# Performance work log

Hardware: AMD Instinct MI355X
Metric: run time of the kernel (lower is better)

Reference implementation:

```python
import jax, jax.numpy as jnp
import numpy as np

EPS = 1e-05
FACT = 2.0
REJECT_RATIO = 1.0
B, N1, N2 = 8, 4096, 4096


def setup_inputs() -> dict:
    key = jax.random.key(0)
    k1, k2 = jax.random.split(key)
    pc1 = jax.random.normal(k1, (B, 4, N1), dtype=jnp.float32)
    pc2 = jax.random.normal(k2, (B, 4, N2), dtype=jnp.float32)
    # homogeneous coordinates: last row is 1
    pc1 = pc1.at[:, 3, :].set(1.0)
    pc2 = pc2.at[:, 3, :].set(1.0)
    return {"pc1": pc1, "pc2": pc2}


def _rot_to_quat(R):
    # quaternion [w, x, y, z] from 3x3 rotation matrix (branchless)
    def s(x):
        return jnp.where(x >= 0, 1.0, -1.0)
    qw = 0.5 * jnp.sqrt(jnp.maximum(1.0 + R[0, 0] + R[1, 1] + R[2, 2], 1e-12))
    qx = 0.5 * jnp.sqrt(jnp.maximum(1.0 + R[0, 0] - R[1, 1] - R[2, 2], 1e-12)) * s(R[2, 1] - R[1, 2])
    qy = 0.5 * jnp.sqrt(jnp.maximum(1.0 - R[0, 0] + R[1, 1] - R[2, 2], 1e-12)) * s(R[0, 2] - R[2, 0])
    qz = 0.5 * jnp.sqrt(jnp.maximum(1.0 - R[0, 0] - R[1, 1] + R[2, 2], 1e-12)) * s(R[1, 0] - R[0, 1])
    return jnp.stack([qw, qx, qy, qz])


def _single(pc1, pc2):
    # pc1: [4, N1], pc2: [4, N2]
    p1, p2 = pc1[:3], pc2[:3]
    # squared pairwise distance via matmul-expansion trick: [N1, N2]
    d = (jnp.sum(p1 ** 2, axis=0)[:, None]
         - 2.0 * jnp.einsum('dn,dm->nm', p1, p2)
         + jnp.sum(p2 ** 2, axis=0)[None, :])
    # soft nearest neighbor: softmax over N2 of fact / clamp(d, eps)
    w = jax.nn.softmax(FACT / jnp.maximum(d, EPS), axis=1)  # [N1, N2]
    pc_nearest = jnp.einsum('cm,nm->cn', pc2, w)            # [4, N1]

    # soft outlier rejection (near-hard threshold via steep sigmoid)
    dist = jnp.linalg.norm(pc1 - pc_nearest, axis=0)        # [N1]
    mean_dist = jnp.mean(dist)
    indexor = jax.nn.sigmoid((dist - mean_dist * REJECT_RATIO - EPS) * -1e10)

    # weighted Procrustes (soft_tf); note indexor weights BOTH centred clouds
    wsum = jnp.sum(indexor)
    c2 = jnp.sum(pc_nearest[:3] * indexor, axis=-1) / wsum  # [3]
    c1 = jnp.sum(pc1[:3] * indexor, axis=-1) / wsum         # [3]
    p2c = ((pc_nearest[:3] - c2[:, None]) * indexor).T      # [N1, 3]
    p1c = ((pc1[:3] - c1[:, None]) * indexor).T             # [N1, 3]
    H = p1c.T @ p2c                                         # [3, 3]
    U, S, Vh = jnp.linalg.svd(H, full_matrices=False)
    V = Vh.T
    sign = jnp.where(jnp.linalg.det(U) * jnp.linalg.det(V) < 0, -1.0, 1.0)
    V = V * jnp.array([1.0, 1.0, 1.0]).at[2].set(sign)[None, :]  # flip 3rd column
    R = V @ U.T
    t = c2 - R @ c1
    T = jnp.zeros((4, 4), dtype=pc1.dtype)
    T = T.at[:3, :3].set(R).at[:3, 3].set(t).at[3, 3].set(1.0)
    q = _rot_to_quat(R)
    return T, q, t


def reference(pc1, pc2):
    T, q, t = jax.vmap(_single)(pc1, pc2)
    return T, q, t
```

## Files before the change

### kernel.cpp

```cpp
#include <hip/hip_runtime.h>
#include <math.h>


typedef float v2f __attribute__((ext_vector_type(2)));

constexpr int cB  = 8;
constexpr int cN1 = 4096;
constexpr int cN2 = 4096;
constexpr int cMC = 8;
constexpr int cCHUNK = cN2 / cMC;
constexpr float cEPS  = 1e-5f;
constexpr float cKK   = 0.34657359027997264f;
constexpr float cEPSK = cEPS * cKK;
constexpr float cUNSC = -1.4426950408889634f;

constexpr size_t OFF_PARTM = 0x400000;
constexpr size_t OFF_NEAR  = 0x500000;

__global__ __launch_bounds__(256) void cpnet_partial(
    const float* __restrict__ pc1, const float* __restrict__ pc2,
    float4* __restrict__ partA, float* __restrict__ partM) {
  __shared__ float xs[cCHUNK], ys[cCHUNK], zs[cCHUNK], ws[cCHUNK];
  const int tid = threadIdx.x;
  const int b = blockIdx.z, c = blockIdx.y;
  const int n = blockIdx.x * 256 + tid;

  const float* p2b = pc2 + (size_t)b * 4 * cN2 + c * cCHUNK;
  for (int i = tid; i < cCHUNK; i += 256) {
    float x = p2b[i], y = p2b[cN2 + i], z = p2b[2 * cN2 + i];
    xs[i] = -2.0f * cKK * x;
    ys[i] = -2.0f * cKK * y;
    zs[i] = -2.0f * cKK * z;
    ws[i] = cKK * (x * x + y * y + z * z);
  }
  __syncthreads();

  const float* p1b = pc1 + (size_t)b * 4 * cN1;
  const float x1 = p1b[n], y1 = p1b[cN1 + n], z1 = p1b[2 * cN1 + n];
  const float n1k = cKK * (x1 * x1 + y1 * y1 + z1 * z1);
  const v2f X1 = {x1, x1}, Y1 = {y1, y1}, Z1 = {z1, z1}, N1K = {n1k, n1k};

  const v2f* xs2 = (const v2f*)xs;
  const v2f* ys2 = (const v2f*)ys;
  const v2f* zs2 = (const v2f*)zs;
  const v2f* ws2 = (const v2f*)ws;

  v2f dmin2 = {3.0e38f, 3.0e38f};
#pragma unroll 4
  for (int m = 0; m < cCHUNK / 2; ++m) {
    v2f dk = X1 * xs2[m] + (Y1 * ys2[m] + (Z1 * zs2[m] + (ws2[m] + N1K)));
    dmin2 = __builtin_elementwise_min(dmin2, dk);
  }
  const float dmin = fminf(dmin2.x, dmin2.y);
  const float M = __builtin_amdgcn_rcpf(fmaxf(dmin, cEPSK));
  const v2f M2 = {M, M};
  const v2f EPS2 = {cEPSK, cEPSK};

  v2f S2 = {0.f, 0.f}, Ax2 = {0.f, 0.f}, Ay2 = {0.f, 0.f}, Az2 = {0.f, 0.f};
#pragma unroll 4
  for (int m = 0; m < cCHUNK / 2; ++m) {
    v2f vx = xs2[m], vy = ys2[m], vz = zs2[m];
    v2f dk = X1 * vx + (Y1 * vy + (Z1 * vz + (ws2[m] + N1K)));
    dk = __builtin_elementwise_max(dk, EPS2);
    v2f s2v;
    s2v.x = __builtin_amdgcn_rcpf(dk.x);
    s2v.y = __builtin_amdgcn_rcpf(dk.y);
    v2f d2 = s2v - M2;
    v2f e;
    e.x = __builtin_amdgcn_exp2f(d2.x);
    e.y = __builtin_amdgcn_exp2f(d2.y);
    S2 += e;
    Ax2 += e * vx;
    Ay2 += e * vy;
    Az2 += e * vz;
  }

  const int idx = (c * cB + b) * cN1 + n;
  partA[idx] = make_float4(Ax2.x + Ax2.y, Ay2.x + Ay2.y, Az2.x + Az2.y,
                           S2.x + S2.y);
  partM[idx] = M;
}

__device__ __forceinline__ void reduce_multi(double* v, int nv, double* lds,
                                             int tid) {
  const int lane = tid & 63, w = tid >> 6;
  for (int i = 0; i < nv; ++i) {
    double x = v[i];
    for (int s = 32; s > 0; s >>= 1) x += __shfl_xor(x, s, 64);
    if (lane == 0) lds[i * 4 + w] = x;
  }
  __syncthreads();
  if (tid < nv)
    lds[tid * 4] = lds[tid * 4] + lds[tid * 4 + 1] + lds[tid * 4 + 2] +
                   lds[tid * 4 + 3];
  __syncthreads();
  for (int i = 0; i < nv; ++i) v[i] = lds[i * 4];
  __syncthreads();
}

__global__ __launch_bounds__(256) void cpnet_finalize(
    const float* __restrict__ pc1,
    const float4* __restrict__ partA, const float* __restrict__ partM,
    float4* __restrict__ near4, float* __restrict__ out) {
  const int b = blockIdx.x, tid = threadIdx.x;
  __shared__ double lds[32 * 4];

  const float* p1b = pc1 + (size_t)b * 4 * cN1;

  double acc[23];
  acc[0] = 0.0;
  for (int n = tid; n < cN1; n += 256) {
    float Ms[cMC];
    float g = -3.0e38f;
#pragma unroll
    for (int c = 0; c < cMC; ++c) {
      Ms[c] = partM[(c * cB + b) * cN1 + n];
      g = fmaxf(g, Ms[c]);
    }
    float S = 0.f, nx = 0.f, ny = 0.f, nz = 0.f;
#pragma unroll
    for (int c = 0; c < cMC; ++c) {
      float w = exp2f(Ms[c] - g);
      float4 a = partA[(c * cB + b) * cN1 + n];
      S += a.w * w; nx += a.x * w; ny += a.y * w; nz += a.z * w;
    }
    float inv = cUNSC / S;
    nx *= inv; ny *= inv; nz *= inv;
    float x1 = p1b[n], y1 = p1b[cN1 + n], z1 = p1b[2 * cN1 + n];
    float dx = x1 - nx, dy = y1 - ny, dz = z1 - nz;
    float dist = sqrtf(dx * dx + dy * dy + dz * dz);
    near4[b * cN1 + n] = make_float4(nx, ny, nz, dist);
    acc[0] += (double)dist;
  }
  reduce_multi(acc, 1, lds, tid);
  const float meanf = (float)(acc[0] / (double)cN1);

  for (int i = 0; i < 23; ++i) acc[i] = 0.0;
  for (int n = tid; n < cN1; n += 256) {
    float4 nn = near4[b * cN1 + n];
    float u = (nn.w - meanf - cEPS) * 1e10f;
    float ind = 1.0f / (1.0f + expf(u));
    double di = (double)ind, di2 = di * di;
    double x1 = (double)p1b[n], y1 = (double)p1b[cN1 + n],
           z1 = (double)p1b[2 * cN1 + n];
    double x2 = (double)nn.x, y2 = (double)nn.y, z2 = (double)nn.z;
    acc[0] += di;
    acc[1] += di * x1;  acc[2] += di * y1;  acc[3] += di * z1;
    acc[4] += di * x2;  acc[5] += di * y2;  acc[6] += di * z2;
    acc[7] += di2;
    acc[8] += di2 * x1;  acc[9] += di2 * y1;  acc[10] += di2 * z1;
    acc[11] += di2 * x2; acc[12] += di2 * y2; acc[13] += di2 * z2;
    acc[14] += di2 * x1 * x2; acc[15] += di2 * x1 * y2; acc[16] += di2 * x1 * z2;
    acc[17] += di2 * y1 * x2; acc[18] += di2 * y1 * y2; acc[19] += di2 * y1 * z2;
    acc[20] += di2 * z1 * x2; acc[21] += di2 * z1 * y2; acc[22] += di2 * z1 * z2;
  }
  reduce_multi(acc, 23, lds, tid);

  if (tid == 0) {
    double W = acc[0];
    double c1[3] = {acc[1] / W, acc[2] / W, acc[3] / W};
    double c2[3] = {acc[4] / W, acc[5] / W, acc[6] / W};
    double H[3][3];
    for (int i = 0; i < 3; ++i)
      for (int j = 0; j < 3; ++j)
        H[i][j] = acc[14 + 3 * i + j] - c2[j] * acc[8 + i] -
                  c1[i] * acc[11 + j] + c1[i] * c2[j] * acc[7];

    double trH = H[0][0] + H[1][1] + H[2][2];
    double Nm[4][4], V[4][4];
    Nm[0][0] = trH;
    Nm[0][1] = Nm[1][0] = H[1][2] - H[2][1];
    Nm[0][2] = Nm[2][0] = H[2][0] - H[0][2];
    Nm[0][3] = Nm[3][0] = H[0][1] - H[1][0];
    Nm[1][1] = 2.0 * H[0][0] - trH;
    Nm[1][2] = Nm[2][1] = H[0][1] + H[1][0];
    Nm[1][3] = Nm[3][1] = H[0][2] + H[2][0];
    Nm[2][2] = 2.0 * H[1][1] - trH;
    Nm[2][3] = Nm[3][2] = H[1][2] + H[2][1];
    Nm[3][3] = 2.0 * H[2][2] - trH;

    for (int i = 0; i < 4; ++i)
      for (int j = 0; j < 4; ++j) V[i][j] = (i == j) ? 1.0 : 0.0;

    for (int sweep = 0; sweep < 6; ++sweep) {
      for (int p = 0; p < 3; ++p) {
        for (int q = p + 1; q < 4; ++q) {
          double apq = Nm[p][q];
          if (fabs(apq) < 1e-300) continue;
          double theta = (Nm[q][q] - Nm[p][p]) / (2.0 * apq);
          double tt = (theta >= 0.0 ? 1.0 : -1.0) /
                      (fabs(theta) + sqrt(theta * theta + 1.0));
          double cc = 1.0 / sqrt(tt * tt + 1.0);
          double ss = tt * cc;
          for (int k = 0; k < 4; ++k) {
            double akp = Nm[k][p], akq = Nm[k][q];
            Nm[k][p] = cc * akp - ss * akq;
            Nm[k][q] = ss * akp + cc * akq;
          }
          for (int k = 0; k < 4; ++k) {
            double apk = Nm[p][k], aqk = Nm[q][k];
            Nm[p][k] = cc * apk - ss * aqk;
            Nm[q][k] = ss * apk + cc * aqk;
          }
          for (int k = 0; k < 4; ++k) {
            double vkp = V[k][p], vkq = V[k][q];
            V[k][p] = cc * vkp - ss * vkq;
            V[k][q] = ss * vkp + cc * vkq;
          }
        }
      }
    }
    int imax = 0;
    for (int i = 1; i < 4; ++i)
      if (Nm[i][i] > Nm[imax][imax]) imax = i;
    double qw = V[0][imax], qx = V[1][imax], qy = V[2][imax], qz = V[3][imax];
    double qn = sqrt(qw * qw + qx * qx + qy * qy + qz * qz);
    qw /= qn; qx /= qn; qy /= qn; qz /= qn;

    double R[3][3];
    R[0][0] = 1.0 - 2.0 * (qy * qy + qz * qz);
    R[0][1] = 2.0 * (qx * qy - qw * qz);
    R[0][2] = 2.0 * (qx * qz + qw * qy);
    R[1][0] = 2.0 * (qx * qy + qw * qz);
    R[1][1] = 1.0 - 2.0 * (qx * qx + qz * qz);
    R[1][2] = 2.0 * (qy * qz - qw * qx);
    R[2][0] = 2.0 * (qx * qz - qw * qy);
    R[2][1] = 2.0 * (qy * qz + qw * qx);
    R[2][2] = 1.0 - 2.0 * (qx * qx + qy * qy);

    double tr1 = 0.0, tr2 = 0.0;
    for (int i = 0; i < 3; ++i)
      for (int j = 0; j < 3; ++j) {
        tr1 += R[i][j] * H[j][i];
        tr2 += R[j][i] * H[j][i];
      }
    if (tr2 > tr1) {
      for (int i = 0; i < 3; ++i)
        for (int j = i + 1; j < 3; ++j) {
          double tmp = R[i][j]; R[i][j] = R[j][i]; R[j][i] = tmp;
        }
    }

    double tx = c2[0] - (R[0][0] * c1[0] + R[0][1] * c1[1] + R[0][2] * c1[2]);
    double ty = c2[1] - (R[1][0] * c1[0] + R[1][1] * c1[1] + R[1][2] * c1[2]);
    double tz = c2[2] - (R[2][0] * c1[0] + R[2][1] * c1[1] + R[2][2] * c1[2]);

    auto sgn = [](double x) { return x >= 0.0 ? 1.0 : -1.0; };
    double oqw = 0.5 * sqrt(fmax(1.0 + R[0][0] + R[1][1] + R[2][2], 1e-12));
    double oqx = 0.5 * sqrt(fmax(1.0 + R[0][0] - R[1][1] - R[2][2], 1e-12)) *
                 sgn(R[2][1] - R[1][2]);
    double oqy = 0.5 * sqrt(fmax(1.0 - R[0][0] + R[1][1] - R[2][2], 1e-12)) *
                 sgn(R[0][2] - R[2][0]);
    double oqz = 0.5 * sqrt(fmax(1.0 - R[0][0] - R[1][1] + R[2][2], 1e-12)) *
                 sgn(R[1][0] - R[0][1]);

    float* T = out + b * 16;
    T[0]  = (float)R[0][0]; T[1]  = (float)R[0][1]; T[2]  = (float)R[0][2]; T[3]  = (float)tx;
    T[4]  = (float)R[1][0]; T[5]  = (float)R[1][1]; T[6]  = (float)R[1][2]; T[7]  = (float)ty;
    T[8]  = (float)R[2][0]; T[9]  = (float)R[2][1]; T[10] = (float)R[2][2]; T[11] = (float)tz;
    T[12] = 0.f; T[13] = 0.f; T[14] = 0.f; T[15] = 1.f;
    float* Q = out + 128 + b * 4;
    Q[0] = (float)oqw; Q[1] = (float)oqx; Q[2] = (float)oqy; Q[3] = (float)oqz;
    float* Tt = out + 160 + b * 3;
    Tt[0] = (float)tx; Tt[1] = (float)ty; Tt[2] = (float)tz;
  }
}

extern "C" void kernel_launch(void* const* d_in, const int* in_sizes, int n_in,
                              void* d_out, int out_size, void* d_ws, size_t ws_size,
                              hipStream_t stream) {
  const float* pc1 = (const float*)d_in[0];
  const float* pc2 = (const float*)d_in[1];
  float* out = (float*)d_out;
  char* ws = (char*)d_ws;

  float4* partA  = (float4*)ws;
  float*  partM  = (float*)(ws + OFF_PARTM);
  float4* near4  = (float4*)(ws + OFF_NEAR);

  cpnet_partial<<<dim3(cN1 / 256, cMC, cB), 256, 0, stream>>>(pc1, pc2,
                                                              partA, partM);
  cpnet_finalize<<<cB, 256, 0, stream>>>(pc1, partA, partM, near4, out);
}
```

Before: 153.3 us.

## Split finalize into parallel combine, moments, and single-thread solve kernels

Replaces the 8-block finalize kernel with three kernels. The first two run on a 16x8 grid and combine the softmax partials and accumulate the weighted moments, each writing per-block partial sums to workspace. A tiny solve kernel then sums those partials and runs the Jacobi eigen solve. This spreads the serial per-batch reduction across many more CUs, at the cost of two extra kernel launches. The combined nearest-point data now overwrites chunk 0 of partA in place.

```diff
diff --git a/kernel.cpp b/kernel.cpp
--- a/kernel.cpp
+++ b/kernel.cpp
@@ -9,13 +9,15 @@
 constexpr int cN2 = 4096;
 constexpr int cMC = 8;
 constexpr int cCHUNK = cN2 / cMC;
+constexpr int cNB2 = cN1 / 256;
 constexpr float cEPS  = 1e-5f;
 constexpr float cKK   = 0.34657359027997264f;
 constexpr float cEPSK = cEPS * cKK;
 constexpr float cUNSC = -1.4426950408889634f;
 
 constexpr size_t OFF_PARTM = 0x400000;
-constexpr size_t OFF_NEAR  = 0x500000;
+constexpr size_t OFF_DPART = 0x500000;
+constexpr size_t OFF_MPART = 0x500400;
 
 __global__ __launch_bounds__(256) void cpnet_partial(
     const float* __restrict__ pc1, const float* __restrict__ pc2,
@@ -98,172 +100,198 @@
   __syncthreads();
 }
 
-__global__ __launch_bounds__(256) void cpnet_finalize(
-    const float* __restrict__ pc1,
-    const float4* __restrict__ partA, const float* __restrict__ partM,
-    float4* __restrict__ near4, float* __restrict__ out) {
-  const int b = blockIdx.x, tid = threadIdx.x;
+__global__ __launch_bounds__(256) void cpnet_combine(
+    const float* __restrict__ pc1, float4* partA,
+    const float* __restrict__ partM, double* __restrict__ dpart) {
   __shared__ double lds[32 * 4];
-
+  const int tid = threadIdx.x;
+  const int bx = blockIdx.x, b = blockIdx.y;
+  const int n = bx * 256 + tid;
+
+  float Ms[cMC];
+  float g = -3.0e38f;
+#pragma unroll
+  for (int c = 0; c < cMC; ++c) {
+    Ms[c] = partM[(c * cB + b) * cN1 + n];
+    g = fmaxf(g, Ms[c]);
+  }
+  float S = 0.f, nx = 0.f, ny = 0.f, nz = 0.f;
+#pragma unroll
+  for (int c = 0; c < cMC; ++c) {
+    float w = exp2f(Ms[c] - g);
+    float4 a = partA[(c * cB + b) * cN1 + n];
+    S += a.w * w; nx += a.x * w; ny += a.y * w; nz += a.z * w;
+  }
+  float inv = cUNSC / S;
+  nx *= inv; ny *= inv; nz *= inv;
   const float* p1b = pc1 + (size_t)b * 4 * cN1;
+  float dx = p1b[n] - nx, dy = p1b[cN1 + n] - ny, dz = p1b[2 * cN1 + n] - nz;
+  float dist = sqrtf(dx * dx + dy * dy + dz * dz);
+  partA[(0 * cB + b) * cN1 + n] = make_float4(nx, ny, nz, dist);
+
+  double acc[1];
+  acc[0] = (double)dist;
+  reduce_multi(acc, 1, lds, tid);
+  if (tid == 0) dpart[b * cNB2 + bx] = acc[0];
+}
+
+__global__ __launch_bounds__(256) void cpnet_moments(
+    const float* __restrict__ pc1, const float4* __restrict__ partA,
+    const double* __restrict__ dpart, double* __restrict__ mpart) {
+  __shared__ double lds[32 * 4];
+  const int tid = threadIdx.x;
+  const int bx = blockIdx.x, b = blockIdx.y;
+  const int n = bx * 256 + tid;
+
+  double dsum = 0.0;
+  for (int i = 0; i < cNB2; ++i) dsum += dpart[b * cNB2 + i];
+  const float meanf = (float)(dsum * (1.0 / (double)cN1));
+
+  float4 nn = partA[(0 * cB + b) * cN1 + n];
+  float u = (nn.w - meanf - cEPS) * 1e10f;
+  float ind = 1.0f / (1.0f + expf(u));
+  const float* p1b = pc1 + (size_t)b * 4 * cN1;
+  double di = (double)ind, di2 = di * di;
+  double x1 = (double)p1b[n], y1 = (double)p1b[cN1 + n],
+         z1 = (double)p1b[2 * cN1 + n];
+  double x2 = (double)nn.x, y2 = (double)nn.y, z2 = (double)nn.z;
+
+  double a[23];
+  a[0] = di;
+  a[1] = di * x1;  a[2] = di * y1;  a[3] = di * z1;
+  a[4] = di * x2;  a[5] = di * y2;  a[6] = di * z2;
+  a[7] = di2;
+  a[8]  = di2 * x1;  a[9]  = di2 * y1;  a[10] = di2 * z1;
+  a[11] = di2 * x2;  a[12] = di2 * y2;  a[13] = di2 * z2;
+  a[14] = di2 * x1 * x2; a[15] = di2 * x1 * y2; a[16] = di2 * x1 * z2;
+  a[17] = di2 * y1 * x2; a[18] = di2 * y1 * y2; a[19] = di2 * y1 * z2;
+  a[20] = di2 * z1 * x2; a[21] = di2 * z1 * y2; a[22] = di2 * z1 * z2;
+
+  reduce_multi(a, 23, lds, tid);
+  if (tid == 0) {
+    double* mb = mpart + (size_t)(b * cNB2 + bx) * 23;
+    for (int i = 0; i < 23; ++i) mb[i] = a[i];
+  }
+}
+
+__global__ __launch_bounds__(64) void cpnet_solve(
+    const double* __restrict__ mpart, float* __restrict__ out) {
+  const int b = blockIdx.x;
+  if (threadIdx.x != 0) return;
 
   double acc[23];
-  acc[0] = 0.0;
-  for (int n = tid; n < cN1; n += 256) {
-    float Ms[cMC];
-    float g = -3.0e38f;
-#pragma unroll
-    for (int c = 0; c < cMC; ++c) {
-      Ms[c] = partM[(c * cB + b) * cN1 + n];
-      g = fmaxf(g, Ms[c]);
-    }
-    float S = 0.f, nx = 0.f, ny = 0.f, nz = 0.f;
-#pragma unroll
-    for (int c = 0; c < cMC; ++c) {
-      float w = exp2f(Ms[c] - g);
-      float4 a = partA[(c * cB + b) * cN1 + n];
-      S += a.w * w; nx += a.x * w; ny += a.y * w; nz += a.z * w;
-    }
-    float inv = cUNSC / S;
-    nx *= inv; ny *= inv; nz *= inv;
-    float x1 = p1b[n], y1 = p1b[cN1 + n], z1 = p1b[2 * cN1 + n];
-    float dx = x1 - nx, dy = y1 - ny, dz = z1 - nz;
-    float dist = sqrtf(dx * dx + dy * dy + dz * dz);
-    near4[b * cN1 + n] = make_float4(nx, ny, nz, dist);
-    acc[0] += (double)dist;
-  }
-  reduce_multi(acc, 1, lds, tid);
-  const float meanf = (float)(acc[0] / (double)cN1);
-
   for (int i = 0; i < 23; ++i) acc[i] = 0.0;
-  for (int n = tid; n < cN1; n += 256) {
-    float4 nn = near4[b * cN1 + n];
-    float u = (nn.w - meanf - cEPS) * 1e10f;
-    float ind = 1.0f / (1.0f + expf(u));
-    double di = (double)ind, di2 = di * di;
-    double x1 = (double)p1b[n], y1 = (double)p1b[cN1 + n],
-           z1 = (double)p1b[2 * cN1 + n];
-    double x2 = (double)nn.x, y2 = (double)nn.y, z2 = (double)nn.z;
-    acc[0] += di;
-    acc[1] += di * x1;  acc[2] += di * y1;  acc[3] += di * z1;
-    acc[4] += di * x2;  acc[5] += di * y2;  acc[6] += di * z2;
-    acc[7] += di2;
-    acc[8] += di2 * x1;  acc[9] += di2 * y1;  acc[10] += di2 * z1;
-    acc[11] += di2 * x2; acc[12] += di2 * y2; acc[13] += di2 * z2;
-    acc[14] += di2 * x1 * x2; acc[15] += di2 * x1 * y2; acc[16] += di2 * x1 * z2;
-    acc[17] += di2 * y1 * x2; acc[18] += di2 * y1 * y2; acc[19] += di2 * y1 * z2;
-    acc[20] += di2 * z1 * x2; acc[21] += di2 * z1 * y2; acc[22] += di2 * z1 * z2;
-  }
-  reduce_multi(acc, 23, lds, tid);
-
-  if (tid == 0) {
-    double W = acc[0];
-    double c1[3] = {acc[1] / W, acc[2] / W, acc[3] / W};
-    double c2[3] = {acc[4] / W, acc[5] / W, acc[6] / W};
-    double H[3][3];
-    for (int i = 0; i < 3; ++i)
-      for (int j = 0; j < 3; ++j)
-        H[i][j] = acc[14 + 3 * i + j] - c2[j] * acc[8 + i] -
-                  c1[i] * acc[11 + j] + c1[i] * c2[j] * acc[7];
-
-    double trH = H[0][0] + H[1][1] + H[2][2];
-    double Nm[4][4], V[4][4];
-    Nm[0][0] = trH;
-    Nm[0][1] = Nm[1][0] = H[1][2] - H[2][1];
-    Nm[0][2] = Nm[2][0] = H[2][0] - H[0][2];
-    Nm[0][3] = Nm[3][0] = H[0][1] - H[1][0];
-    Nm[1][1] = 2.0 * H[0][0] - trH;
-    Nm[1][2] = Nm[2][1] = H[0][1] + H[1][0];
-    Nm[1][3] = Nm[3][1] = H[0][2] + H[2][0];
-    Nm[2][2] = 2.0 * H[1][1] - trH;
-    Nm[2][3] = Nm[3][2] = H[1][2] + H[2][1];
-    Nm[3][3] = 2.0 * H[2][2] - trH;
-
-    for (int i = 0; i < 4; ++i)
-      for (int j = 0; j < 4; ++j) V[i][j] = (i == j) ? 1.0 : 0.0;
-
-    for (int sweep = 0; sweep < 6; ++sweep) {
-      for (int p = 0; p < 3; ++p) {
-        for (int q = p + 1; q < 4; ++q) {
-          double apq = Nm[p][q];
-          if (fabs(apq) < 1e-300) continue;
-          double theta = (Nm[q][q] - Nm[p][p]) / (2.0 * apq);
-          double tt = (theta >= 0.0 ? 1.0 : -1.0) /
-                      (fabs(theta) + sqrt(theta * theta + 1.0));
-          double cc = 1.0 / sqrt(tt * tt + 1.0);
-          double ss = tt * cc;
-          for (int k = 0; k < 4; ++k) {
-            double akp = Nm[k][p], akq = Nm[k][q];
-            Nm[k][p] = cc * akp - ss * akq;
-            Nm[k][q] = ss * akp + cc * akq;
-          }
-          for (int k = 0; k < 4; ++k) {
-            double apk = Nm[p][k], aqk = Nm[q][k];
-            Nm[p][k] = cc * apk - ss * aqk;
-            Nm[q][k] = ss * apk + cc * aqk;
-          }
-          for (int k = 0; k < 4; ++k) {
-            double vkp = V[k][p], vkq = V[k][q];
-            V[k][p] = cc * vkp - ss * vkq;
-            V[k][q] = ss * vkp + cc * vkq;
-          }
+  for (int k = 0; k < cNB2; ++k) {
+    const double* mb = mpart + (size_t)(b * cNB2 + k) * 23;
+    for (int i = 0; i < 23; ++i) acc[i] += mb[i];
+  }
+
+  double W = acc[0];
+  double c1[3] = {acc[1] / W, acc[2] / W, acc[3] / W};
+  double c2[3] = {acc[4] / W, acc[5] / W, acc[6] / W};
+  double H[3][3];
+  for (int i = 0; i < 3; ++i)
+    for (int j = 0; j < 3; ++j)
+      H[i][j] = acc[14 + 3 * i + j] - c2[j] * acc[8 + i] -
+                c1[i] * acc[11 + j] + c1[i] * c2[j] * acc[7];
+
+  double trH = H[0][0] + H[1][1] + H[2][2];
+  double Nm[4][4], V[4][4];
+  Nm[0][0] = trH;
+  Nm[0][1] = Nm[1][0] = H[1][2] - H[2][1];
+  Nm[0][2] = Nm[2][0] = H[2][0] - H[0][2];
+  Nm[0][3] = Nm[3][0] = H[0][1] - H[1][0];
+  Nm[1][1] = 2.0 * H[0][0] - trH;
+  Nm[1][2] = Nm[2][1] = H[0][1] + H[1][0];
+  Nm[1][3] = Nm[3][1] = H[0][2] + H[2][0];
+  Nm[2][2] = 2.0 * H[1][1] - trH;
+  Nm[2][3] = Nm[3][2] = H[1][2] + H[2][1];
+  Nm[3][3] = 2.0 * H[2][2] - trH;
+
+  for (int i = 0; i < 4; ++i)
+    for (int j = 0; j < 4; ++j) V[i][j] = (i == j) ? 1.0 : 0.0;
+
+  for (int sweep = 0; sweep < 6; ++sweep) {
+    for (int p = 0; p < 3; ++p) {
+      for (int q = p + 1; q < 4; ++q) {
+        double apq = Nm[p][q];
+        if (fabs(apq) < 1e-300) continue;
+        double theta = (Nm[q][q] - Nm[p][p]) / (2.0 * apq);
+        double tt = (theta >= 0.0 ? 1.0 : -1.0) /
+                    (fabs(theta) + sqrt(theta * theta + 1.0));
+        double cc = 1.0 / sqrt(tt * tt + 1.0);
+        double ss = tt * cc;
+        for (int k = 0; k < 4; ++k) {
+          double akp = Nm[k][p], akq = Nm[k][q];
+          Nm[k][p] = cc * akp - ss * akq;
+          Nm[k][q] = ss * akp + cc * akq;
+        }
+        for (int k = 0; k < 4; ++k) {
+          double apk = Nm[p][k], aqk = Nm[q][k];
+          Nm[p][k] = cc * apk - ss * aqk;
+          Nm[q][k] = ss * apk + cc * aqk;
+        }
+        for (int k = 0; k < 4; ++k) {
+          double vkp = V[k][p], vkq = V[k][q];
+          V[k][p] = cc * vkp - ss * vkq;
+          V[k][q] = ss * vkp + cc * vkq;
         }
       }
     }
-    int imax = 0;
-    for (int i = 1; i < 4; ++i)
-      if (Nm[i][i] > Nm[imax][imax]) imax = i;
-    double qw = V[0][imax], qx = V[1][imax], qy = V[2][imax], qz = V[3][imax];
-    double qn = sqrt(qw * qw + qx * qx + qy * qy + qz * qz);
-    qw /= qn; qx /= qn; qy /= qn; qz /= qn;
-
-    double R[3][3];
-    R[0][0] = 1.0 - 2.0 * (qy * qy + qz * qz);
-    R[0][1] = 2.0 * (qx * qy - qw * qz);
-    R[0][2] = 2.0 * (qx * qz + qw * qy);
-    R[1][0] = 2.0 * (qx * qy + qw * qz);
-    R[1][1] = 1.0 - 2.0 * (qx * qx + qz * qz);
-    R[1][2] = 2.0 * (qy * qz - qw * qx);
-    R[2][0] = 2.0 * (qx * qz - qw * qy);
-    R[2][1] = 2.0 * (qy * qz + qw * qx);
-    R[2][2] = 1.0 - 2.0 * (qx * qx + qy * qy);
-
-    double tr1 = 0.0, tr2 = 0.0;
+  }
+  int imax = 0;
+  for (int i = 1; i < 4; ++i)
+    if (Nm[i][i] > Nm[imax][imax]) imax = i;
+  double qw = V[0][imax], qx = V[1][imax], qy = V[2][imax], qz = V[3][imax];
+  double qn = sqrt(qw * qw + qx * qx + qy * qy + qz * qz);
+  qw /= qn; qx /= qn; qy /= qn; qz /= qn;
+
+  double R[3][3];
+  R[0][0] = 1.0 - 2.0 * (qy * qy + qz * qz);
+  R[0][1] = 2.0 * (qx * qy - qw * qz);
+  R[0][2] = 2.0 * (qx * qz + qw * qy);
+  R[1][0] = 2.0 * (qx * qy + qw * qz);
+  R[1][1] = 1.0 - 2.0 * (qx * qx + qz * qz);
+  R[1][2] = 2.0 * (qy * qz - qw * qx);
+  R[2][0] = 2.0 * (qx * qz - qw * qy);
+  R[2][1] = 2.0 * (qy * qz + qw * qx);
+  R[2][2] = 1.0 - 2.0 * (qx * qx + qy * qy);
+
+  double tr1 = 0.0, tr2 = 0.0;
+  for (int i = 0; i < 3; ++i)
+    for (int j = 0; j < 3; ++j) {
+      tr1 += R[i][j] * H[j][i];
+      tr2 += R[j][i] * H[j][i];
+    }
+  if (tr2 > tr1) {
     for (int i = 0; i < 3; ++i)
-      for (int j = 0; j < 3; ++j) {
-        tr1 += R[i][j] * H[j][i];
-        tr2 += R[j][i] * H[j][i];
+      for (int j = i + 1; j < 3; ++j) {
+        double tmp = R[i][j]; R[i][j] = R[j][i]; R[j][i] = tmp;
       }
-    if (tr2 > tr1) {
-      for (int i = 0; i < 3; ++i)
-        for (int j = i + 1; j < 3; ++j) {
-          double tmp = R[i][j]; R[i][j] = R[j][i]; R[j][i] = tmp;
-        }
-    }
-
-    double tx = c2[0] - (R[0][0] * c1[0] + R[0][1] * c1[1] + R[0][2] * c1[2]);
-    double ty = c2[1] - (R[1][0] * c1[0] + R[1][1] * c1[1] + R[1][2] * c1[2]);
-    double tz = c2[2] - (R[2][0] * c1[0] + R[2][1] * c1[1] + R[2][2] * c1[2]);
-
-    auto sgn = [](double x) { return x >= 0.0 ? 1.0 : -1.0; };
-    double oqw = 0.5 * sqrt(fmax(1.0 + R[0][0] + R[1][1] + R[2][2], 1e-12));
-    double oqx = 0.5 * sqrt(fmax(1.0 + R[0][0] - R[1][1] - R[2][2], 1e-12)) *
-                 sgn(R[2][1] - R[1][2]);
-    double oqy = 0.5 * sqrt(fmax(1.0 - R[0][0] + R[1][1] - R[2][2], 1e-12)) *
-                 sgn(R[0][2] - R[2][0]);
-    double oqz = 0.5 * sqrt(fmax(1.0 - R[0][0] - R[1][1] + R[2][2], 1e-12)) *
-                 sgn(R[1][0] - R[0][1]);
-
-    float* T = out + b * 16;
-    T[0]  = (float)R[0][0]; T[1]  = (float)R[0][1]; T[2]  = (float)R[0][2]; T[3]  = (float)tx;
-    T[4]  = (float)R[1][0]; T[5]  = (float)R[1][1]; T[6]  = (float)R[1][2]; T[7]  = (float)ty;
-    T[8]  = (float)R[2][0]; T[9]  = (float)R[2][1]; T[10] = (float)R[2][2]; T[11] = (float)tz;
-    T[12] = 0.f; T[13] = 0.f; T[14] = 0.f; T[15] = 1.f;
-    float* Q = out + 128 + b * 4;
-    Q[0] = (float)oqw; Q[1] = (float)oqx; Q[2] = (float)oqy; Q[3] = (float)oqz;
-    float* Tt = out + 160 + b * 3;
-    Tt[0] = (float)tx; Tt[1] = (float)ty; Tt[2] = (float)tz;
-  }
+  }
+
+  double tx = c2[0] - (R[0][0] * c1[0] + R[0][1] * c1[1] + R[0][2] * c1[2]);
+  double ty = c2[1] - (R[1][0] * c1[0] + R[1][1] * c1[1] + R[1][2] * c1[2]);
+  double tz = c2[2] - (R[2][0] * c1[0] + R[2][1] * c1[1] + R[2][2] * c1[2]);
+
+  auto sgn = [](double x) { return x >= 0.0 ? 1.0 : -1.0; };
+  double oqw = 0.5 * sqrt(fmax(1.0 + R[0][0] + R[1][1] + R[2][2], 1e-12));
+  double oqx = 0.5 * sqrt(fmax(1.0 + R[0][0] - R[1][1] - R[2][2], 1e-12)) *
+               sgn(R[2][1] - R[1][2]);
+  double oqy = 0.5 * sqrt(fmax(1.0 - R[0][0] + R[1][1] - R[2][2], 1e-12)) *
+               sgn(R[0][2] - R[2][0]);
+  double oqz = 0.5 * sqrt(fmax(1.0 - R[0][0] - R[1][1] + R[2][2], 1e-12)) *
+               sgn(R[1][0] - R[0][1]);
+
+  float* T = out + b * 16;
+  T[0]  = (float)R[0][0]; T[1]  = (float)R[0][1]; T[2]  = (float)R[0][2]; T[3]  = (float)tx;
+  T[4]  = (float)R[1][0]; T[5]  = (float)R[1][1]; T[6]  = (float)R[1][2]; T[7]  = (float)ty;
+  T[8]  = (float)R[2][0]; T[9]  = (float)R[2][1]; T[10] = (float)R[2][2]; T[11] = (float)tz;
+  T[12] = 0.f; T[13] = 0.f; T[14] = 0.f; T[15] = 1.f;
+  float* Q = out + 128 + b * 4;
+  Q[0] = (float)oqw; Q[1] = (float)oqx; Q[2] = (float)oqy; Q[3] = (float)oqz;
+  float* Tt = out + 160 + b * 3;
+  Tt[0] = (float)tx; Tt[1] = (float)ty; Tt[2] = (float)tz;
 }
 
 extern "C" void kernel_launch(void* const* d_in, const int* in_sizes, int n_in,
@@ -274,11 +302,14 @@
   float* out = (float*)d_out;
   char* ws = (char*)d_ws;
 
-  float4* partA  = (float4*)ws;
-  float*  partM  = (float*)(ws + OFF_PARTM);
-  float4* near4  = (float4*)(ws + OFF_NEAR);
+  float4* partA = (float4*)ws;
+  float*  partM = (float*)(ws + OFF_PARTM);
+  double* dpart = (double*)(ws + OFF_DPART);
+  double* mpart = (double*)(ws + OFF_MPART);
 
   cpnet_partial<<<dim3(cN1 / 256, cMC, cB), 256, 0, stream>>>(pc1, pc2,
                                                               partA, partM);
-  cpnet_finalize<<<cB, 256, 0, stream>>>(pc1, partA, partM, near4, out);
-}
+  cpnet_combine<<<dim3(cNB2, cB), 256, 0, stream>>>(pc1, partA, partM, dpart);
+  cpnet_moments<<<dim3(cNB2, cB), 256, 0, stream>>>(pc1, partA, dpart, mpart);
+  cpnet_solve<<<cB, 64, 0, stream>>>(mpart, out);
+}
```

New measurement: 142.7 us. 1.07x faster.

## Fuse partial and finalize kernels using last-block-done atomic counter per batch

Applied to the files above, without the earlier changes.

Merges the two kernels into one: each block computes its partial softmax sums, then atomically increments a per-batch counter, and the last block for each batch performs the finalize reduction and Procrustes solve. This removes a kernel launch and the global barrier between the stages, and lets a batch finalize while other batches are still computing. It adds a memset launch for the counters, and the finalize work is still done by a single block per batch at the tail.

```diff
diff --git a/kernel.cpp b/kernel.cpp
--- a/kernel.cpp
+++ b/kernel.cpp
@@ -9,6 +9,8 @@
 constexpr int cN2 = 4096;
 constexpr int cMC = 8;
 constexpr int cCHUNK = cN2 / cMC;
+constexpr int cNB = cN1 / 256;
+constexpr int cBLK = cNB * cMC;
 constexpr float cEPS  = 1e-5f;
 constexpr float cKK   = 0.34657359027997264f;
 constexpr float cEPSK = cEPS * cKK;
@@ -16,70 +18,7 @@
 
 constexpr size_t OFF_PARTM = 0x400000;
 constexpr size_t OFF_NEAR  = 0x500000;
-
-__global__ __launch_bounds__(256) void cpnet_partial(
-    const float* __restrict__ pc1, const float* __restrict__ pc2,
-    float4* __restrict__ partA, float* __restrict__ partM) {
-  __shared__ float xs[cCHUNK], ys[cCHUNK], zs[cCHUNK], ws[cCHUNK];
-  const int tid = threadIdx.x;
-  const int b = blockIdx.z, c = blockIdx.y;
-  const int n = blockIdx.x * 256 + tid;
-
-  const float* p2b = pc2 + (size_t)b * 4 * cN2 + c * cCHUNK;
-  for (int i = tid; i < cCHUNK; i += 256) {
-    float x = p2b[i], y = p2b[cN2 + i], z = p2b[2 * cN2 + i];
-    xs[i] = -2.0f * cKK * x;
-    ys[i] = -2.0f * cKK * y;
-    zs[i] = -2.0f * cKK * z;
-    ws[i] = cKK * (x * x + y * y + z * z);
-  }
-  __syncthreads();
-
-  const float* p1b = pc1 + (size_t)b * 4 * cN1;
-  const float x1 = p1b[n], y1 = p1b[cN1 + n], z1 = p1b[2 * cN1 + n];
-  const float n1k = cKK * (x1 * x1 + y1 * y1 + z1 * z1);
-  const v2f X1 = {x1, x1}, Y1 = {y1, y1}, Z1 = {z1, z1}, N1K = {n1k, n1k};
-
-  const v2f* xs2 = (const v2f*)xs;
-  const v2f* ys2 = (const v2f*)ys;
-  const v2f* zs2 = (const v2f*)zs;
-  const v2f* ws2 = (const v2f*)ws;
-
-  v2f dmin2 = {3.0e38f, 3.0e38f};
-#pragma unroll 4
-  for (int m = 0; m < cCHUNK / 2; ++m) {
-    v2f dk = X1 * xs2[m] + (Y1 * ys2[m] + (Z1 * zs2[m] + (ws2[m] + N1K)));
-    dmin2 = __builtin_elementwise_min(dmin2, dk);
-  }
-  const float dmin = fminf(dmin2.x, dmin2.y);
-  const float M = __builtin_amdgcn_rcpf(fmaxf(dmin, cEPSK));
-  const v2f M2 = {M, M};
-  const v2f EPS2 = {cEPSK, cEPSK};
-
-  v2f S2 = {0.f, 0.f}, Ax2 = {0.f, 0.f}, Ay2 = {0.f, 0.f}, Az2 = {0.f, 0.f};
-#pragma unroll 4
-  for (int m = 0; m < cCHUNK / 2; ++m) {
-    v2f vx = xs2[m], vy = ys2[m], vz = zs2[m];
-    v2f dk = X1 * vx + (Y1 * vy + (Z1 * vz + (ws2[m] + N1K)));
-    dk = __builtin_elementwise_max(dk, EPS2);
-    v2f s2v;
-    s2v.x = __builtin_amdgcn_rcpf(dk.x);
-    s2v.y = __builtin_amdgcn_rcpf(dk.y);
-    v2f d2 = s2v - M2;
-    v2f e;
-    e.x = __builtin_amdgcn_exp2f(d2.x);
-    e.y = __builtin_amdgcn_exp2f(d2.y);
-    S2 += e;
-    Ax2 += e * vx;
-    Ay2 += e * vy;
-    Az2 += e * vz;
-  }
-
-  const int idx = (c * cB + b) * cN1 + n;
-  partA[idx] = make_float4(Ax2.x + Ax2.y, Ay2.x + Ay2.y, Az2.x + Az2.y,
-                           S2.x + S2.y);
-  partM[idx] = M;
-}
+constexpr size_t OFF_CNT   = 0x580000;
 
 __device__ __forceinline__ void reduce_multi(double* v, int nv, double* lds,
                                              int tid) {
@@ -98,58 +37,127 @@
   __syncthreads();
 }
 
-__global__ __launch_bounds__(256) void cpnet_finalize(
-    const float* __restrict__ pc1,
-    const float4* __restrict__ partA, const float* __restrict__ partM,
-    float4* __restrict__ near4, float* __restrict__ out) {
-  const int b = blockIdx.x, tid = threadIdx.x;
+__global__ __launch_bounds__(256) void cpnet_fused(
+    const float* __restrict__ pc1, const float* __restrict__ pc2,
+    float4* __restrict__ partA, float* __restrict__ partM,
+    float4* __restrict__ near4, unsigned int* __restrict__ cnt,
+    float* __restrict__ out) {
+  __shared__ float xs[cCHUNK], ys[cCHUNK], zs[cCHUNK], ws[cCHUNK];
   __shared__ double lds[32 * 4];
+  __shared__ int is_last;
+  const int tid = threadIdx.x;
+  const int nb = blockIdx.x, c = blockIdx.y, b = blockIdx.z;
+  const int n = nb * 256 + tid;
+
+  {
+    const float* p2b = pc2 + (size_t)b * 4 * cN2 + c * cCHUNK;
+    for (int i = tid; i < cCHUNK; i += 256) {
+      float x = p2b[i], y = p2b[cN2 + i], z = p2b[2 * cN2 + i];
+      xs[i] = -2.0f * cKK * x;
+      ys[i] = -2.0f * cKK * y;
+      zs[i] = -2.0f * cKK * z;
+      ws[i] = cKK * (x * x + y * y + z * z);
+    }
+    __syncthreads();
+
+    const float* p1b = pc1 + (size_t)b * 4 * cN1;
+    const float x1 = p1b[n], y1 = p1b[cN1 + n], z1 = p1b[2 * cN1 + n];
+    const float n1k = cKK * (x1 * x1 + y1 * y1 + z1 * z1);
+    const v2f X1 = {x1, x1}, Y1 = {y1, y1}, Z1 = {z1, z1}, N1K = {n1k, n1k};
+
+    const v2f* xs2 = (const v2f*)xs;
+    const v2f* ys2 = (const v2f*)ys;
+    const v2f* zs2 = (const v2f*)zs;
+    const v2f* ws2 = (const v2f*)ws;
+
+    v2f dmin2 = {3.0e38f, 3.0e38f};
+#pragma unroll 4
+    for (int m = 0; m < cCHUNK / 2; ++m) {
+      v2f dk = X1 * xs2[m] + (Y1 * ys2[m] + (Z1 * zs2[m] + (ws2[m] + N1K)));
+      dmin2 = __builtin_elementwise_min(dmin2, dk);
+    }
+    const float dmin = fminf(dmin2.x, dmin2.y);
+    const float M = __builtin_amdgcn_rcpf(fmaxf(dmin, cEPSK));
+    const v2f M2 = {M, M};
+    const v2f EPS2 = {cEPSK, cEPSK};
+
+    v2f S2 = {0.f, 0.f}, Ax2 = {0.f, 0.f}, Ay2 = {0.f, 0.f}, Az2 = {0.f, 0.f};
+#pragma unroll 4
+    for (int m = 0; m < cCHUNK / 2; ++m) {
+      v2f vx = xs2[m], vy = ys2[m], vz = zs2[m];
+      v2f dk = X1 * vx + (Y1 * vy + (Z1 * vz + (ws2[m] + N1K)));
+      dk = __builtin_elementwise_max(dk, EPS2);
+      v2f s2v;
+      s2v.x = __builtin_amdgcn_rcpf(dk.x);
+      s2v.y = __builtin_amdgcn_rcpf(dk.y);
+      v2f d2 = s2v - M2;
+      v2f e;
+      e.x = __builtin_amdgcn_exp2f(d2.x);
+      e.y = __builtin_amdgcn_exp2f(d2.y);
+      S2 += e;
+      Ax2 += e * vx;
+      Ay2 += e * vy;
+      Az2 += e * vz;
+    }
+
+    const int idx = (c * cB + b) * cN1 + n;
+    partA[idx] = make_float4(Ax2.x + Ax2.y, Ay2.x + Ay2.y, Az2.x + Az2.y,
+                             S2.x + S2.y);
+    partM[idx] = M;
+  }
+
+  __threadfence();
+  if (tid == 0)
+    is_last = (atomicAdd(&cnt[b], 1u) == (unsigned)(cBLK - 1));
+  __syncthreads();
+  if (!is_last) return;
+  __threadfence();
 
   const float* p1b = pc1 + (size_t)b * 4 * cN1;
 
   double acc[23];
   acc[0] = 0.0;
-  for (int n = tid; n < cN1; n += 256) {
+  for (int n2 = tid; n2 < cN1; n2 += 256) {
     float Ms[cMC];
     float g = -3.0e38f;
 #pragma unroll
-    for (int c = 0; c < cMC; ++c) {
-      Ms[c] = partM[(c * cB + b) * cN1 + n];
-      g = fmaxf(g, Ms[c]);
+    for (int c2 = 0; c2 < cMC; ++c2) {
+      Ms[c2] = partM[(c2 * cB + b) * cN1 + n2];
+      g = fmaxf(g, Ms[c2]);
     }
     float S = 0.f, nx = 0.f, ny = 0.f, nz = 0.f;
 #pragma unroll
-    for (int c = 0; c < cMC; ++c) {
-      float w = exp2f(Ms[c] - g);
-      float4 a = partA[(c * cB + b) * cN1 + n];
+    for (int c2 = 0; c2 < cMC; ++c2) {
+      float w = exp2f(Ms[c2] - g);
+      float4 a = partA[(c2 * cB + b) * cN1 + n2];
       S += a.w * w; nx += a.x * w; ny += a.y * w; nz += a.z * w;
     }
     float inv = cUNSC / S;
     nx *= inv; ny *= inv; nz *= inv;
-    float x1 = p1b[n], y1 = p1b[cN1 + n], z1 = p1b[2 * cN1 + n];
-    float dx = x1 - nx, dy = y1 - ny, dz = z1 - nz;
+    float xx1 = p1b[n2], yy1 = p1b[cN1 + n2], zz1 = p1b[2 * cN1 + n2];
+    float dx = xx1 - nx, dy = yy1 - ny, dz = zz1 - nz;
     float dist = sqrtf(dx * dx + dy * dy + dz * dz);
-    near4[b * cN1 + n] = make_float4(nx, ny, nz, dist);
+    near4[b * cN1 + n2] = make_float4(nx, ny, nz, dist);
     acc[0] += (double)dist;
   }
   reduce_multi(acc, 1, lds, tid);
   const float meanf = (float)(acc[0] / (double)cN1);
 
   for (int i = 0; i < 23; ++i) acc[i] = 0.0;
-  for (int n = tid; n < cN1; n += 256) {
-    float4 nn = near4[b * cN1 + n];
+  for (int n2 = tid; n2 < cN1; n2 += 256) {
+    float4 nn = near4[b * cN1 + n2];
     float u = (nn.w - meanf - cEPS) * 1e10f;
     float ind = 1.0f / (1.0f + expf(u));
     double di = (double)ind, di2 = di * di;
-    double x1 = (double)p1b[n], y1 = (double)p1b[cN1 + n],
-           z1 = (double)p1b[2 * cN1 + n];
+    double x1 = (double)p1b[n2], y1 = (double)p1b[cN1 + n2],
+           z1 = (double)p1b[2 * cN1 + n2];
     double x2 = (double)nn.x, y2 = (double)nn.y, z2 = (double)nn.z;
     acc[0] += di;
     acc[1] += di * x1;  acc[2] += di * y1;  acc[3] += di * z1;
     acc[4] += di * x2;  acc[5] += di * y2;  acc[6] += di * z2;
     acc[7] += di2;
-    acc[8] += di2 * x1;  acc[9] += di2 * y1;  acc[10] += di2 * z1;
-    acc[11] += di2 * x2; acc[12] += di2 * y2; acc[13] += di2 * z2;
+    acc[8]  += di2 * x1;  acc[9]  += di2 * y1;  acc[10] += di2 * z1;
+    acc[11] += di2 * x2;  acc[12] += di2 * y2;  acc[13] += di2 * z2;
     acc[14] += di2 * x1 * x2; acc[15] += di2 * x1 * y2; acc[16] += di2 * x1 * z2;
     acc[17] += di2 * y1 * x2; acc[18] += di2 * y1 * y2; acc[19] += di2 * y1 * z2;
     acc[20] += di2 * z1 * x2; acc[21] += di2 * z1 * y2; acc[22] += di2 * z1 * z2;
@@ -274,11 +282,12 @@
   float* out = (float*)d_out;
   char* ws = (char*)d_ws;
 
-  float4* partA  = (float4*)ws;
-  float*  partM  = (float*)(ws + OFF_PARTM);
-  float4* near4  = (float4*)(ws + OFF_NEAR);
-
-  cpnet_partial<<<dim3(cN1 / 256, cMC, cB), 256, 0, stream>>>(pc1, pc2,
-                                                              partA, partM);
-  cpnet_finalize<<<cB, 256, 0, stream>>>(pc1, partA, partM, near4, out);
+  float4* partA = (float4*)ws;
+  float*  partM = (float*)(ws + OFF_PARTM);
+  float4* near4 = (float4*)(ws + OFF_NEAR);
+  unsigned int* cnt = (unsigned int*)(ws + OFF_CNT);
+
+  hipMemsetAsync(cnt, 0, cB * sizeof(unsigned int), stream);
+  cpnet_fused<<<dim3(cNB, cMC, cB), 256, 0, stream>>>(pc1, pc2, partA, partM,
+                                                      near4, cnt, out);
 }
```

New measurement: 233.8 us. +52.5%, slower.
